# Kernel optimization log

Hardware: AMD Instinct MI355X
Metric: run time of the kernel (lower is better)

Reference implementation:

```python
import jax, jax.numpy as jnp
import numpy as np

D_MODEL = 1024
N_HEADS = 16
D_K = D_MODEL // N_HEADS  # 64
THETA = 10000.0
MAX_SEQ_LEN = 2048
GPT_INIT_STD = 0.02


def _apply_rope(x, token_positions):
    """x: (b, h, t, d_k); token_positions: (b_or_1, t) int.
    Even/odd interleaved rotation, matching the torch RoPE module."""
    d_half = D_K // 2
    j = jnp.arange(d_half, dtype=jnp.float32)
    inv_freq = THETA ** (-2.0 * j / float(D_K))              # (d_half,)
    angles = token_positions.astype(jnp.float32)[..., None] * inv_freq  # (b, t, d_half)
    cos = jnp.cos(angles)[:, None, :, :].astype(x.dtype)     # (b, 1, t, d_half)
    sin = jnp.sin(angles)[:, None, :, :].astype(x.dtype)
    x_even = x[..., 0::2]
    x_odd = x[..., 1::2]
    r_even = x_even * cos - x_odd * sin
    r_odd = x_even * sin + x_odd * cos
    return jnp.stack([r_even, r_odd], axis=-1).reshape(x.shape)


def setup_inputs() -> dict:
    key = jax.random.key(0)
    kx, kq, kk, kv, ko = jax.random.split(key, 5)
    B, T = 2, 2048
    x = jax.random.normal(kx, (B, T, D_MODEL), dtype=jnp.float32)
    # torch nn.Linear stores weight as (out_features, in_features); y = x @ W.T
    Wq = (jax.random.normal(kq, (D_MODEL, D_MODEL), dtype=jnp.float32) * GPT_INIT_STD)
    Wk = (jax.random.normal(kk, (D_MODEL, D_MODEL), dtype=jnp.float32) * GPT_INIT_STD)
    Wv = (jax.random.normal(kv, (D_MODEL, D_MODEL), dtype=jnp.float32) * GPT_INIT_STD)
    Wo = (jax.random.normal(ko, (D_MODEL, D_MODEL), dtype=jnp.float32) * GPT_INIT_STD)
    token_positions = jnp.arange(T, dtype=jnp.int32)[None, :]  # (1, T), monotonic
    return {"x": x, "Wq": Wq, "Wk": Wk, "Wv": Wv, "Wo": Wo,
            "token_positions": token_positions}


def reference(x, Wq, Wk, Wv, Wo, token_positions):
    B, T, _ = x.shape
    # QKV projections (bias-free linear, torch convention y = x @ W.T)
    Q = (x @ Wq.T).reshape(B, T, N_HEADS, D_K).transpose(0, 2, 1, 3)  # (b,h,t,d)
    K = (x @ Wk.T).reshape(B, T, N_HEADS, D_K).transpose(0, 2, 1, 3)
    V = (x @ Wv.T).reshape(B, T, N_HEADS, D_K).transpose(0, 2, 1, 3)

    Q = _apply_rope(Q, token_positions)
    K = _apply_rope(K, token_positions)

    scaling = 1.0 / np.sqrt(D_K).astype(np.float32)
    scores = jnp.einsum('bhqd,bhkd->bhqk', Q, K) * scaling    # (b,h,t,t)
    # causal mask: key position <= query position (positions are monotonic)
    qp = token_positions  # (1 or b, t)
    causal = qp[:, None, :] <= qp[:, :, None]                 # (b_or_1, t, t)
    causal = causal[:, None, :, :]                            # (b_or_1, 1, t, t)
    neg = jnp.finfo(scores.dtype).min
    scores = jnp.where(causal, scores, neg)
    attn = jax.nn.softmax(scores.astype(jnp.float32), axis=-1).astype(x.dtype)
    out = jnp.einsum('bhqk,bhkd->bhqd', attn, V)              # (b,h,t,d)
    out = out.transpose(0, 2, 1, 3).reshape(B, T, D_MODEL)
    return out @ Wo.T
```

## Files before the change

kernel.cpp:

```cpp
#include <hip/hip_runtime.h>
#include <hip/hip_bf16.h>

typedef __attribute__((ext_vector_type(8))) __bf16 bf16x8;
typedef __attribute__((ext_vector_type(4))) __bf16 bf16x4;
typedef __attribute__((ext_vector_type(4))) float f32x4;

#define T_SEQ   2048
#define DMODEL  1024

__device__ __forceinline__ void gload_lds16(const void* g, void* l) {
  __builtin_amdgcn_global_load_lds((const __attribute__((address_space(1))) void*)g,
                                   (__attribute__((address_space(3))) void*)l, 16, 0, 0);
}
#define VMCNT0() asm volatile("s_waitcnt vmcnt(0)" ::: "memory")

__global__ __launch_bounds__(256) void f32_to_bf16_k(const float* __restrict__ s,
                                                     __bf16* __restrict__ d, int n) {
  int i = (blockIdx.x * 256 + threadIdx.x) * 8;
  if (i >= n) return;
  float4 a = *(const float4*)(s + i);
  float4 b = *(const float4*)(s + i + 4);
  bf16x8 o;
  o[0] = (__bf16)a.x; o[1] = (__bf16)a.y; o[2] = (__bf16)a.z; o[3] = (__bf16)a.w;
  o[4] = (__bf16)b.x; o[5] = (__bf16)b.y; o[6] = (__bf16)b.z; o[7] = (__bf16)b.w;
  *(bf16x8*)(d + i) = o;
}

__global__ __launch_bounds__(256) void w_to_bf16_k(const float* __restrict__ Wq,
                                                   const float* __restrict__ Wk,
                                                   const float* __restrict__ Wv,
                                                   const float* __restrict__ Wo,
                                                   __bf16* __restrict__ wqkv,
                                                   __bf16* __restrict__ wob) {
  int i = (blockIdx.x * 256 + threadIdx.x) * 8;
  int sec = i >> 20, o = i & 1048575;
  const float* s = (sec == 0) ? Wq : (sec == 1) ? Wk : (sec == 2) ? Wv : Wo;
  __bf16* d = (sec == 3) ? (wob + o) : (wqkv + i);
  float4 a = *(const float4*)(s + o);
  float4 b = *(const float4*)(s + o + 4);
  bf16x8 v;
  v[0] = (__bf16)a.x; v[1] = (__bf16)a.y; v[2] = (__bf16)a.z; v[3] = (__bf16)a.w;
  v[4] = (__bf16)b.x; v[5] = (__bf16)b.y; v[6] = (__bf16)b.z; v[7] = (__bf16)b.w;
  *(bf16x8*)d = v;
}

__global__ __launch_bounds__(256) void rope_table_k(const int* __restrict__ pos,
                                                    float2* __restrict__ tbl) {
  int idx = blockIdx.x * 256 + threadIdx.x;
  int t = idx >> 5, j = idx & 31;
  float p = (float)pos[t];
  float inv = powf(10000.0f, -(float)j * (1.0f / 32.0f));
  float a = p * inv;
  tbl[idx] = make_float2(cosf(a), sinf(a));
}

template <typename OutT>
__global__ __launch_bounds__(256) void gemm_bt(const __bf16* __restrict__ A,
                                               const __bf16* __restrict__ W,
                                               OutT* __restrict__ C,
                                               int M, int N, int K) {
  __shared__ alignas(16) __bf16 At[128 * 32];
  __shared__ alignas(16) __bf16 Bt[128 * 32];
  const int tid = threadIdx.x, w = tid >> 6, l = tid & 63;
  const int l16 = l & 15, lq = l >> 4;
  const int wm = w >> 1, wn = w & 1;
  const int br = blockIdx.y * 128, bc = blockIdx.x * 128;
  f32x4 acc[4][4] = {};
  const int off = w * 1024 + l * 16;
  const int rA = off >> 6, cA = off & 63;

  for (int kt = 0; kt < K; kt += 32) {
    __syncthreads();
    gload_lds16((const char*)A + ((size_t)(br + rA) * K + kt) * 2 + cA,
                (char*)At + w * 1024);
    gload_lds16((const char*)A + ((size_t)(br + 64 + rA) * K + kt) * 2 + cA,
                (char*)At + 4096 + w * 1024);
    gload_lds16((const char*)W + ((size_t)(bc + rA) * K + kt) * 2 + cA,
                (char*)Bt + w * 1024);
    gload_lds16((const char*)W + ((size_t)(bc + 64 + rA) * K + kt) * 2 + cA,
                (char*)Bt + 4096 + w * 1024);
    __syncthreads();

    bf16x8 af[4], bfr[4];
#pragma unroll
    for (int m = 0; m < 4; ++m)
      af[m] = *(const bf16x8*)(At + (wm * 64 + m * 16 + l16) * 32 + lq * 8);
#pragma unroll
    for (int n = 0; n < 4; ++n)
      bfr[n] = *(const bf16x8*)(Bt + (wn * 64 + n * 16 + l16) * 32 + lq * 8);
#pragma unroll
    for (int m = 0; m < 4; ++m)
#pragma unroll
      for (int n = 0; n < 4; ++n)
        acc[m][n] = __builtin_amdgcn_mfma_f32_16x16x32_bf16(af[m], bfr[n], acc[m][n], 0, 0, 0);
  }

#pragma unroll
  for (int m = 0; m < 4; ++m)
#pragma unroll
    for (int n = 0; n < 4; ++n)
#pragma unroll
      for (int r = 0; r < 4; ++r) {
        int row = br + wm * 64 + m * 16 + lq * 4 + r;
        int col = bc + wn * 64 + n * 16 + l16;
        float v = acc[m][n][r];
        if constexpr (__is_same(OutT, float))
          C[(size_t)row * N + col] = v;
        else
          C[(size_t)row * N + col] = (__bf16)v;
      }
}

__global__ __launch_bounds__(256) void gemm_qkv_k(const __bf16* __restrict__ A,
                                                  const __bf16* __restrict__ W,
                                                  __bf16* __restrict__ qr,
                                                  __bf16* __restrict__ kr,
                                                  __bf16* __restrict__ vt,
                                                  const float2* __restrict__ tbl) {
  __shared__ alignas(16) __bf16 At[128 * 32];
  __shared__ alignas(16) __bf16 Bt[128 * 32];
  const int K = 1024;
  const int tid = threadIdx.x, w = tid >> 6, l = tid & 63;
  const int l16 = l & 15, lq = l >> 4;
  const int wm = w >> 1, wn = w & 1;
  const int br = blockIdx.y * 128, bc = blockIdx.x * 128;
  f32x4 acc[4][4] = {};
  const int off = w * 1024 + l * 16;
  const int rA = off >> 6, cA = off & 63;

  for (int kt = 0; kt < K; kt += 32) {
    __syncthreads();
    gload_lds16((const char*)A + ((size_t)(br + rA) * K + kt) * 2 + cA,
                (char*)At + w * 1024);
    gload_lds16((const char*)A + ((size_t)(br + 64 + rA) * K + kt) * 2 + cA,
                (char*)At + 4096 + w * 1024);
    gload_lds16((const char*)W + ((size_t)(bc + rA) * K + kt) * 2 + cA,
                (char*)Bt + w * 1024);
    gload_lds16((const char*)W + ((size_t)(bc + 64 + rA) * K + kt) * 2 + cA,
                (char*)Bt + 4096 + w * 1024);
    __syncthreads();

    bf16x8 af[4], bfr[4];
#pragma unroll
    for (int m = 0; m < 4; ++m)
      af[m] = *(const bf16x8*)(At + (wm * 64 + m * 16 + l16) * 32 + lq * 8);
#pragma unroll
    for (int n = 0; n < 4; ++n)
      bfr[n] = *(const bf16x8*)(Bt + (wn * 64 + n * 16 + l16) * 32 + lq * 8);
#pragma unroll
    for (int n = 0; n < 4; ++n)
#pragma unroll
      for (int m = 0; m < 4; ++m)
        acc[n][m] = __builtin_amdgcn_mfma_f32_16x16x32_bf16(bfr[n], af[m], acc[n][m], 0, 0, 0);
  }

  const int sec = bc >> 10;
  const int cb = bc & 1023;
  if (sec == 2) {
#pragma unroll
    for (int n = 0; n < 4; ++n)
#pragma unroll
      for (int m = 0; m < 4; ++m) {
        int d0 = cb + wn * 64 + n * 16 + lq * 4;
        int h = d0 >> 6, dk = d0 & 63;
        int t = br + wm * 64 + m * 16 + l16;
        int b = t >> 11, tt = t & 2047;
#pragma unroll
        for (int r = 0; r < 4; ++r)
          vt[((size_t)((b * 16 + h) * 64 + dk + r)) * T_SEQ + tt] = (__bf16)acc[n][m][r];
      }
  } else {
    __bf16* dst = (sec == 0) ? qr : kr;
    const float sc = (sec == 0) ? 0.125f : 1.0f;
#pragma unroll
    for (int n = 0; n < 4; ++n)
#pragma unroll
      for (int m = 0; m < 4; ++m) {
        int d0 = cb + wn * 64 + n * 16 + lq * 4;
        int h = d0 >> 6, dk = d0 & 63;
        int t = br + wm * 64 + m * 16 + l16;
        int b = t >> 11, tt = t & 2047;
        float2 cs0 = tbl[tt * 32 + (dk >> 1)];
        float2 cs1 = tbl[tt * 32 + (dk >> 1) + 1];
        float v0 = acc[n][m][0], v1 = acc[n][m][1];
        float v2 = acc[n][m][2], v3 = acc[n][m][3];
        bf16x4 pk;
        pk[0] = (__bf16)((v0 * cs0.x - v1 * cs0.y) * sc);
        pk[1] = (__bf16)((v0 * cs0.y + v1 * cs0.x) * sc);
        pk[2] = (__bf16)((v2 * cs1.x - v3 * cs1.y) * sc);
        pk[3] = (__bf16)((v2 * cs1.y + v3 * cs1.x) * sc);
        *(bf16x4*)(dst + ((size_t)((b * 16 + h) * T_SEQ + tt)) * 64 + dk) = pk;
      }
  }
}

__global__ __launch_bounds__(256) void attn_k(const __bf16* __restrict__ Qr,
                                              const __bf16* __restrict__ Kr,
                                              const __bf16* __restrict__ Vt,
                                              __bf16* __restrict__ out) {
  __shared__ alignas(16) __bf16 Kt[2][64 * 64];
  __shared__ alignas(16) __bf16 Vtl[2][64 * 64];
  __shared__ alignas(16) __bf16 Pt[4][16 * 64];
  const int bh = blockIdx.x, qb0 = blockIdx.y * 64;
  const int tid = threadIdx.x, w = tid >> 6, l = tid & 63;
  const int l16 = l & 15, lq = l >> 4;
  const int px = (l16 & 7) << 4;

  const __bf16* Qbase = Qr + ((size_t)bh * T_SEQ + qb0 + w * 16) * 64;
  bf16x8 aq0 = *(const bf16x8*)(Qbase + l16 * 64 + lq * 8);
  bf16x8 aq1 = *(const bf16x8*)(Qbase + l16 * 64 + 32 + lq * 8);

  float mrow = -1e30f, lrow = 0.0f;
  f32x4 acc[4] = {};

  const int nt = qb0 / 64 + 1;
  const int offbase = w * 1024 + l * 16;

  auto stage = [&](int bufi, int kt) {
#pragma unroll
    for (int c2 = 0; c2 < 2; ++c2) {
      int o = offbase + c2 * 4096;
      int row = o >> 7, cbyte = o & 127;
      int sw = cbyte ^ ((row & 7) << 4);
      gload_lds16((const char*)Kr + ((size_t)(bh * T_SEQ + kt + row) * 64) * 2 + sw,
                  (char*)(&Kt[bufi][0]) + w * 1024 + c2 * 4096);
      gload_lds16((const char*)Vt + ((size_t)(bh * 64 + row) * T_SEQ + kt) * 2 + sw,
                  (char*)(&Vtl[bufi][0]) + w * 1024 + c2 * 4096);
    }
  };

  stage(0, 0);
  VMCNT0();
  __builtin_amdgcn_s_barrier();

  int buf = 0;
  for (int t = 0; t < nt; ++t) {
    const int kt = t * 64;
    if (t + 1 < nt) stage(buf ^ 1, kt + 64);

    const char* K0 = (const char*)&Kt[buf][0];
    const char* V0 = (const char*)&Vtl[buf][0];

    f32x4 s[4] = {};
    __builtin_amdgcn_s_setprio(1);
#pragma unroll
    for (int g = 0; g < 4; ++g) {
      int row = g * 16 + l16;
      int x = (row & 7) << 4;
      bf16x8 k0 = *(const bf16x8*)(K0 + row * 128 + ((lq * 16) ^ x));
      s[g] = __builtin_amdgcn_mfma_f32_16x16x32_bf16(k0, aq0, s[g], 0, 0, 0);
      bf16x8 k1 = *(const bf16x8*)(K0 + row * 128 + ((lq * 16 + 64) ^ x));
      s[g] = __builtin_amdgcn_mfma_f32_16x16x32_bf16(k1, aq1, s[g], 0, 0, 0);
    }
    __builtin_amdgcn_s_setprio(0);

    if (t == nt - 1) {
      int q = qb0 + w * 16 + l16;
#pragma unroll
      for (int g = 0; g < 4; ++g)
#pragma unroll
        for (int r = 0; r < 4; ++r)
          if (kt + g * 16 + lq * 4 + r > q) s[g][r] = -1e30f;
    }

    float pm = -1e30f;
#pragma unroll
    for (int g = 0; g < 4; ++g)
#pragma unroll
      for (int r = 0; r < 4; ++r) pm = fmaxf(pm, s[g][r]);
    pm = fmaxf(pm, __shfl_xor(pm, 16));
    pm = fmaxf(pm, __shfl_xor(pm, 32));

    if (__any(pm > mrow + 8.0f)) {
      float mn = fmaxf(mrow, pm);
      float alpha = __expf(mrow - mn);
#pragma unroll
      for (int dt = 0; dt < 4; ++dt)
#pragma unroll
        for (int r = 0; r < 4; ++r) acc[dt][r] *= alpha;
      lrow *= alpha;
      mrow = mn;
    }

    char* Pw = (char*)&Pt[w][0] + l16 * 128;
    float rs = 0.0f;
#pragma unroll
    for (int g = 0; g < 4; ++g) {
      bf16x4 pk;
#pragma unroll
      for (int r = 0; r < 4; ++r) {
        float p = __expf(s[g][r] - mrow);
        rs += p;
        pk[r] = (__bf16)p;
      }
      *(bf16x4*)(Pw + ((g * 32 + lq * 8) ^ px)) = pk;
    }
    rs += __shfl_xor(rs, 16);
    rs += __shfl_xor(rs, 32);
    lrow += rs;

    __builtin_amdgcn_s_setprio(1);
#pragma unroll
    for (int ks = 0; ks < 2; ++ks) {
      bf16x8 ap = *(const bf16x8*)((const char*)&Pt[w][0] + l16 * 128 +
                                   ((ks * 64 + lq * 16) ^ px));
#pragma unroll
      for (int dt = 0; dt < 4; ++dt) {
        int vrow = dt * 16 + l16;
        bf16x8 vf = *(const bf16x8*)(V0 + vrow * 128 +
                                     ((ks * 64 + lq * 16) ^ ((vrow & 7) << 4)));
        acc[dt] = __builtin_amdgcn_mfma_f32_16x16x32_bf16(vf, ap, acc[dt], 0, 0, 0);
      }
    }
    __builtin_amdgcn_s_setprio(0);

    VMCNT0();
    __builtin_amdgcn_s_barrier();
    buf ^= 1;
  }

  const int b = bh >> 4, h = bh & 15;
  float inv = 1.0f / lrow;
  size_t row = (size_t)b * T_SEQ + qb0 + w * 16 + l16;
#pragma unroll
  for (int dt = 0; dt < 4; ++dt) {
    bf16x4 o;
#pragma unroll
    for (int r = 0; r < 4; ++r) o[r] = (__bf16)(acc[dt][r] * inv);
    *(bf16x4*)(out + row * DMODEL + h * 64 + dt * 16 + lq * 4) = o;
  }
}

extern "C" void kernel_launch(void* const* d_in, const int* in_sizes, int n_in,
                              void* d_out, int out_size, void* d_ws, size_t ws_size,
                              hipStream_t stream) {
  const float* x  = (const float*)d_in[0];
  const float* Wq = (const float*)d_in[1];
  const float* Wk = (const float*)d_in[2];
  const float* Wv = (const float*)d_in[3];
  const float* Wo = (const float*)d_in[4];
  const int* pos  = (const int*)d_in[5];

  char* ws = (char*)d_ws;
  __bf16* xb   = (__bf16*)(ws + 0);
  __bf16* wqkv = (__bf16*)(ws + (8u << 20));
  __bf16* wob  = (__bf16*)(ws + (14u << 20));
  __bf16* qr   = (__bf16*)(ws + (16u << 20));
  __bf16* kr   = (__bf16*)(ws + (24u << 20));
  __bf16* vt   = (__bf16*)(ws + (32u << 20));
  __bf16* ao   = (__bf16*)(ws + (40u << 20));
  float2* tbl  = (float2*)(ws + (48u << 20));

  f32_to_bf16_k<<<2048, 256, 0, stream>>>(x, xb, 4194304);
  w_to_bf16_k<<<2048, 256, 0, stream>>>(Wq, Wk, Wv, Wo, wqkv, wob);
  rope_table_k<<<256, 256, 0, stream>>>(pos, tbl);

  gemm_qkv_k<<<dim3(24, 32), 256, 0, stream>>>(xb, wqkv, qr, kr, vt, tbl);

  attn_k<<<dim3(32, 32), 256, 0, stream>>>(qr, kr, vt, ao);

  gemm_bt<float><<<dim3(8, 32), 256, 0, stream>>>(ao, wob, (float*)d_out, 4096, DMODEL, DMODEL);
}
```

Measured before the change: 218.3 us.

## Double-buffer GEMM LDS tiles, swizzle block order across XCDs, reverse attention order

Both GEMMs now use two LDS buffers, issuing the next K-tile's global-to-LDS loads before the MFMAs on the current tile, with one barrier per iteration and setprio around the MFMA block. All three main kernels move to 1D grids with an XCD-aware block swizzle, which is meant to improve L2 locality. Attention processes the longest causal query blocks first to balance load. The RoPE table is transposed to position-major per frequency, so table reads in the QKV epilogue are coalesced across lanes. LDS use doubles, which may reduce occupancy.

```diff
diff --git a/kernel.cpp b/kernel.cpp
--- a/kernel.cpp
+++ b/kernel.cpp
@@ -47,7 +47,7 @@
 __global__ __launch_bounds__(256) void rope_table_k(const int* __restrict__ pos,
                                                     float2* __restrict__ tbl) {
   int idx = blockIdx.x * 256 + threadIdx.x;
-  int t = idx >> 5, j = idx & 31;
+  int j = idx >> 11, t = idx & 2047;
   float p = (float)pos[t];
   float inv = powf(10000.0f, -(float)j * (1.0f / 32.0f));
   float a = p * inv;
@@ -59,40 +59,57 @@
                                                const __bf16* __restrict__ W,
                                                OutT* __restrict__ C,
                                                int M, int N, int K) {
-  __shared__ alignas(16) __bf16 At[128 * 32];
-  __shared__ alignas(16) __bf16 Bt[128 * 32];
+  __shared__ alignas(16) __bf16 At[2][128 * 32];
+  __shared__ alignas(16) __bf16 Bt[2][128 * 32];
   const int tid = threadIdx.x, w = tid >> 6, l = tid & 63;
   const int l16 = l & 15, lq = l >> 4;
   const int wm = w >> 1, wn = w & 1;
-  const int br = blockIdx.y * 128, bc = blockIdx.x * 128;
+  const int nwg = gridDim.x, chunk = nwg >> 3, f = blockIdx.x;
+  const int swz = (f & 7) * chunk + (f >> 3);
+  const int nx = N >> 7;
+  const int br = (swz / nx) * 128, bc = (swz % nx) * 128;
   f32x4 acc[4][4] = {};
   const int off = w * 1024 + l * 16;
   const int rA = off >> 6, cA = off & 63;
 
-  for (int kt = 0; kt < K; kt += 32) {
-    __syncthreads();
+  auto stage = [&](int bufi, int kt) {
     gload_lds16((const char*)A + ((size_t)(br + rA) * K + kt) * 2 + cA,
-                (char*)At + w * 1024);
+                (char*)(&At[bufi][0]) + w * 1024);
     gload_lds16((const char*)A + ((size_t)(br + 64 + rA) * K + kt) * 2 + cA,
-                (char*)At + 4096 + w * 1024);
+                (char*)(&At[bufi][0]) + 4096 + w * 1024);
     gload_lds16((const char*)W + ((size_t)(bc + rA) * K + kt) * 2 + cA,
-                (char*)Bt + w * 1024);
+                (char*)(&Bt[bufi][0]) + w * 1024);
     gload_lds16((const char*)W + ((size_t)(bc + 64 + rA) * K + kt) * 2 + cA,
-                (char*)Bt + 4096 + w * 1024);
-    __syncthreads();
+                (char*)(&Bt[bufi][0]) + 4096 + w * 1024);
+  };
+
+  stage(0, 0);
+  VMCNT0();
+  __builtin_amdgcn_s_barrier();
+
+  const int nkt = K >> 5;
+  int buf = 0;
+  for (int i = 0; i < nkt; ++i) {
+    if (i + 1 < nkt) stage(buf ^ 1, (i + 1) << 5);
 
     bf16x8 af[4], bfr[4];
 #pragma unroll
     for (int m = 0; m < 4; ++m)
-      af[m] = *(const bf16x8*)(At + (wm * 64 + m * 16 + l16) * 32 + lq * 8);
-#pragma unroll
-    for (int n = 0; n < 4; ++n)
-      bfr[n] = *(const bf16x8*)(Bt + (wn * 64 + n * 16 + l16) * 32 + lq * 8);
+      af[m] = *(const bf16x8*)(&At[buf][0] + (wm * 64 + m * 16 + l16) * 32 + lq * 8);
+#pragma unroll
+    for (int n = 0; n < 4; ++n)
+      bfr[n] = *(const bf16x8*)(&Bt[buf][0] + (wn * 64 + n * 16 + l16) * 32 + lq * 8);
+    __builtin_amdgcn_s_setprio(1);
 #pragma unroll
     for (int m = 0; m < 4; ++m)
 #pragma unroll
       for (int n = 0; n < 4; ++n)
         acc[m][n] = __builtin_amdgcn_mfma_f32_16x16x32_bf16(af[m], bfr[n], acc[m][n], 0, 0, 0);
+    __builtin_amdgcn_s_setprio(0);
+
+    VMCNT0();
+    __builtin_amdgcn_s_barrier();
+    buf ^= 1;
   }
 
 #pragma unroll
@@ -117,41 +134,56 @@
                                                   __bf16* __restrict__ kr,
                                                   __bf16* __restrict__ vt,
                                                   const float2* __restrict__ tbl) {
-  __shared__ alignas(16) __bf16 At[128 * 32];
-  __shared__ alignas(16) __bf16 Bt[128 * 32];
+  __shared__ alignas(16) __bf16 At[2][128 * 32];
+  __shared__ alignas(16) __bf16 Bt[2][128 * 32];
   const int K = 1024;
   const int tid = threadIdx.x, w = tid >> 6, l = tid & 63;
   const int l16 = l & 15, lq = l >> 4;
   const int wm = w >> 1, wn = w & 1;
-  const int br = blockIdx.y * 128, bc = blockIdx.x * 128;
+  const int f = blockIdx.x;
+  const int swz = (f & 7) * 96 + (f >> 3);
+  const int br = (swz / 24) * 128, bc = (swz % 24) * 128;
   f32x4 acc[4][4] = {};
   const int off = w * 1024 + l * 16;
   const int rA = off >> 6, cA = off & 63;
 
-  for (int kt = 0; kt < K; kt += 32) {
-    __syncthreads();
+  auto stage = [&](int bufi, int kt) {
     gload_lds16((const char*)A + ((size_t)(br + rA) * K + kt) * 2 + cA,
-                (char*)At + w * 1024);
+                (char*)(&At[bufi][0]) + w * 1024);
     gload_lds16((const char*)A + ((size_t)(br + 64 + rA) * K + kt) * 2 + cA,
-                (char*)At + 4096 + w * 1024);
+                (char*)(&At[bufi][0]) + 4096 + w * 1024);
     gload_lds16((const char*)W + ((size_t)(bc + rA) * K + kt) * 2 + cA,
-                (char*)Bt + w * 1024);
+                (char*)(&Bt[bufi][0]) + w * 1024);
     gload_lds16((const char*)W + ((size_t)(bc + 64 + rA) * K + kt) * 2 + cA,
-                (char*)Bt + 4096 + w * 1024);
-    __syncthreads();
+                (char*)(&Bt[bufi][0]) + 4096 + w * 1024);
+  };
+
+  stage(0, 0);
+  VMCNT0();
+  __builtin_amdgcn_s_barrier();
+
+  int buf = 0;
+  for (int i = 0; i < 32; ++i) {
+    if (i + 1 < 32) stage(buf ^ 1, (i + 1) << 5);
 
     bf16x8 af[4], bfr[4];
 #pragma unroll
     for (int m = 0; m < 4; ++m)
-      af[m] = *(const bf16x8*)(At + (wm * 64 + m * 16 + l16) * 32 + lq * 8);
-#pragma unroll
-    for (int n = 0; n < 4; ++n)
-      bfr[n] = *(const bf16x8*)(Bt + (wn * 64 + n * 16 + l16) * 32 + lq * 8);
+      af[m] = *(const bf16x8*)(&At[buf][0] + (wm * 64 + m * 16 + l16) * 32 + lq * 8);
+#pragma unroll
+    for (int n = 0; n < 4; ++n)
+      bfr[n] = *(const bf16x8*)(&Bt[buf][0] + (wn * 64 + n * 16 + l16) * 32 + lq * 8);
+    __builtin_amdgcn_s_setprio(1);
 #pragma unroll
     for (int n = 0; n < 4; ++n)
 #pragma unroll
       for (int m = 0; m < 4; ++m)
         acc[n][m] = __builtin_amdgcn_mfma_f32_16x16x32_bf16(bfr[n], af[m], acc[n][m], 0, 0, 0);
+    __builtin_amdgcn_s_setprio(0);
+
+    VMCNT0();
+    __builtin_amdgcn_s_barrier();
+    buf ^= 1;
   }
 
   const int sec = bc >> 10;
@@ -180,8 +212,8 @@
         int h = d0 >> 6, dk = d0 & 63;
         int t = br + wm * 64 + m * 16 + l16;
         int b = t >> 11, tt = t & 2047;
-        float2 cs0 = tbl[tt * 32 + (dk >> 1)];
-        float2 cs1 = tbl[tt * 32 + (dk >> 1) + 1];
+        float2 cs0 = tbl[(dk >> 1) * T_SEQ + tt];
+        float2 cs1 = tbl[((dk >> 1) + 1) * T_SEQ + tt];
         float v0 = acc[n][m][0], v1 = acc[n][m][1];
         float v2 = acc[n][m][2], v3 = acc[n][m][3];
         bf16x4 pk;
@@ -201,7 +233,10 @@
   __shared__ alignas(16) __bf16 Kt[2][64 * 64];
   __shared__ alignas(16) __bf16 Vtl[2][64 * 64];
   __shared__ alignas(16) __bf16 Pt[4][16 * 64];
-  const int bh = blockIdx.x, qb0 = blockIdx.y * 64;
+  const int f = blockIdx.x;
+  const int swz = (f & 7) * 128 + (f >> 3);
+  const int bh = swz >> 5;
+  const int qb0 = (31 - (swz & 31)) * 64;
   const int tid = threadIdx.x, w = tid >> 6, l = tid & 63;
   const int l16 = l & 15, lq = l >> 4;
   const int px = (l16 & 7) << 4;
@@ -355,9 +390,9 @@
   w_to_bf16_k<<<2048, 256, 0, stream>>>(Wq, Wk, Wv, Wo, wqkv, wob);
   rope_table_k<<<256, 256, 0, stream>>>(pos, tbl);
 
-  gemm_qkv_k<<<dim3(24, 32), 256, 0, stream>>>(xb, wqkv, qr, kr, vt, tbl);
-
-  attn_k<<<dim3(32, 32), 256, 0, stream>>>(qr, kr, vt, ao);
-
-  gemm_bt<float><<<dim3(8, 32), 256, 0, stream>>>(ao, wob, (float*)d_out, 4096, DMODEL, DMODEL);
-}
+  gemm_qkv_k<<<768, 256, 0, stream>>>(xb, wqkv, qr, kr, vt, tbl);
+
+  attn_k<<<1024, 256, 0, stream>>>(qr, kr, vt, ao);
+
+  gemm_bt<float><<<256, 256, 0, stream>>>(ao, wob, (float*)d_out, 4096, DMODEL, DMODEL);
+}
```

Result: slower. 230.6 us (+5.6%).
